# Kernel optimization log

Hardware: AMD Instinct MI355X
Metric: run time of the kernel (lower is better)

## Reference

```python
import jax, jax.numpy as jnp
import numpy as np

N = 50000      # nodes
E = 600000     # edges (avg degree 12)
D_IN = 16      # node_input_size
D = 128        # hidden_size
H = 4          # num_heads
DH = D // H
L = 4          # message_passing_num
D_FF = 512     # 4*hidden FFN expansion
D_OUT = 3      # output_size


def setup_inputs() -> dict:
    key = jax.random.key(0)
    ks = iter(jax.random.split(key, 32))
    def w(shape, fan_in):
        return jax.random.normal(next(ks), shape, jnp.float32) / np.float32(np.sqrt(fan_in))
    return {
        "features": jax.random.normal(next(ks), (N, D_IN), jnp.float32),
        "senders": jax.random.randint(next(ks), (E,), 0, N),
        "receivers": jax.random.randint(next(ks), (E,), 0, N),
        "enc_w1": w((D_IN, D), D_IN), "enc_b1": jnp.zeros((D,), jnp.float32),
        "enc_w2": w((D, D), D),       "enc_b2": jnp.zeros((D,), jnp.float32),
        "wq": w((L, D, D), D), "wk": w((L, D, D), D),
        "wv": w((L, D, D), D), "wo": w((L, D, D), D),
        "ln1_s": jnp.ones((L, D), jnp.float32), "ln1_b": jnp.zeros((L, D), jnp.float32),
        "ffn_w1": w((L, D, D_FF), D), "ffn_b1": jnp.zeros((L, D_FF), jnp.float32),
        "ffn_w2": w((L, D_FF, D), D_FF), "ffn_b2": jnp.zeros((L, D), jnp.float32),
        "ln2_s": jnp.ones((L, D), jnp.float32), "ln2_b": jnp.zeros((L, D), jnp.float32),
        "dec_w1": w((D, D_OUT), D), "dec_b1": jnp.zeros((D_OUT,), jnp.float32),
        "dec_w2": w((D_OUT, D_OUT), D_OUT), "dec_b2": jnp.zeros((D_OUT,), jnp.float32),
    }


def _ln(x, s, b):
    mu = x.mean(-1, keepdims=True)
    var = ((x - mu) ** 2).mean(-1, keepdims=True)
    return (x - mu) * jax.lax.rsqrt(var + 1e-5) * s + b


def _graph_mha(x, senders, receivers, wq, wk, wv, wo):
    # Adjacency-masked attention done sparsely over the edge list
    # (equivalent to softmax over the BCOO adjacency pattern).
    n = x.shape[0]
    q = (x @ wq).reshape(n, H, DH)
    k = (x @ wk).reshape(n, H, DH)
    v = (x @ wv).reshape(n, H, DH)
    scores = (q[receivers] * k[senders]).sum(-1) / np.float32(np.sqrt(DH))  # [E,H]
    m = jax.ops.segment_max(scores, receivers, num_segments=n)             # [N,H]
    m = jnp.where(jnp.isfinite(m), m, 0.0)
    a = jnp.exp(scores - m[receivers])                                      # [E,H]
    denom = jax.ops.segment_sum(a, receivers, num_segments=n)              # [N,H]
    msg = jax.ops.segment_sum(a[:, :, None] * v[senders], receivers, num_segments=n)  # [N,H,DH]
    out = (msg / (denom[:, :, None] + 1e-9)).reshape(n, D)
    return out @ wo


def reference(features, senders, receivers,
              enc_w1, enc_b1, enc_w2, enc_b2,
              wq, wk, wv, wo, ln1_s, ln1_b,
              ffn_w1, ffn_b1, ffn_w2, ffn_b2, ln2_s, ln2_b,
              dec_w1, dec_b1, dec_w2, dec_b2):
    # encode
    x = jnp.maximum(features @ enc_w1 + enc_b1, 0.0) @ enc_w2 + enc_b2     # [N,D]
    # process: L pre-LN sparse-attention transformer blocks
    for l in range(L):
        h = _ln(x, ln1_s[l], ln1_b[l])
        x = x + _graph_mha(h, senders, receivers, wq[l], wk[l], wv[l], wo[l])
        h = _ln(x, ln2_s[l], ln2_b[l])
        x = x + jnp.maximum(h @ ffn_w1[l] + ffn_b1[l], 0.0) @ ffn_w2[l] + ffn_b2[l]
    # decode
    return jnp.maximum(x @ dec_w1 + dec_b1, 0.0) @ dec_w2 + dec_b2         # [N,D_OUT]
```

## Files before the change

kernel.cpp:

```cpp
#include <hip/hip_runtime.h>
#include <hip/hip_bf16.h>
#include <math.h>

#define D     128
#define NHEAD 4
#define DH    32
#define DFF   512
#define DIN   16
#define MAXDEG 64
#define TN    16

typedef __attribute__((ext_vector_type(8))) short bf16x8;
typedef __attribute__((ext_vector_type(4))) float f32x4;
typedef __hip_bfloat16 bf16;

#define QSCALE_L2E 0.2550348838f

#define BMQ 128

#define WAITV(N) asm volatile("s_waitcnt vmcnt(" #N ")" ::: "memory")
#define WAITLGKM asm volatile("s_waitcnt lgkmcnt(0)" ::: "memory")
#define FENCE()  asm volatile("" ::: "memory")
#define BAR() do { FENCE(); __builtin_amdgcn_s_barrier(); FENCE(); } while (0)

__device__ __forceinline__ void gll16(const bf16* g, bf16* l) {
    __builtin_amdgcn_global_load_lds((__attribute__((address_space(1))) void*)g,
                                     (__attribute__((address_space(3))) void*)l,
                                     16, 0, 0);
}

__device__ __forceinline__ ushort bfbits(float f) {
    __hip_bfloat16 b = __float2bfloat16(f);
    return *(ushort*)&b;
}

__global__ void k_fill(const int* __restrict__ recv, const int* __restrict__ senders,
                       int* __restrict__ deg, int* __restrict__ eid, int E) {
    int e = blockIdx.x * blockDim.x + threadIdx.x;
    if (e >= E) return;
    int r = recv[e];
    int pos = atomicAdd(&deg[r], 1);
    if (pos < MAXDEG) eid[r * MAXDEG + pos] = senders[e];
}

__global__ void k_wt(const float* __restrict__ wq, const float* __restrict__ wk,
                     const float* __restrict__ wv, const float* __restrict__ wo,
                     const float* __restrict__ w1, const float* __restrict__ w2,
                     const float* __restrict__ encw2,
                     bf16* __restrict__ wqkvT, bf16* __restrict__ woT,
                     bf16* __restrict__ w1T, bf16* __restrict__ w2T,
                     bf16* __restrict__ encw2T, int* __restrict__ deg,
                     int* __restrict__ eid, int N) {
    int r = blockIdx.y;
    if (r == 25) {
        int tot = N + N * MAXDEG;
        for (int i = blockIdx.x * blockDim.x + threadIdx.x; i < tot;
             i += 256 * 256) {
            if (i < N) deg[i] = 0;
            else eid[i - N] = 0;
        }
        return;
    }
    const float* src; bf16* dst; int K, Nout;
    if (r < 12) {
        int l = r / 3, sel = r % 3;
        src = (sel == 0 ? wq : sel == 1 ? wk : wv) + (size_t)l * D * D;
        dst = wqkvT + (size_t)l * 3 * D * D + (size_t)sel * D * D;
        K = D; Nout = D;
    } else if (r < 16) {
        int l = r - 12;
        src = wo + (size_t)l * D * D; dst = woT + (size_t)l * D * D; K = D; Nout = D;
    } else if (r < 20) {
        int l = r - 16;
        src = w1 + (size_t)l * D * DFF; dst = w1T + (size_t)l * D * DFF; K = D; Nout = DFF;
    } else if (r < 24) {
        int l = r - 20;
        src = w2 + (size_t)l * DFF * D; dst = w2T + (size_t)l * DFF * D; K = DFF; Nout = D;
    } else {
        src = encw2; dst = encw2T; K = D; Nout = D;
    }
    int total = K * Nout;
    int i = blockIdx.x * blockDim.x + threadIdx.x;
    if (i >= total) return;
    int k = i / Nout, j = i % Nout;
    dst[(size_t)j * K + k] = __float2bfloat16(src[i]);
}

__device__ __forceinline__ void load_afrag(const bf16* A, int arow, int quad,
                                           int N, bf16x8* afr) {
    const bf16* ab = A + (size_t)arow * D + quad * 8;
#pragma unroll
    for (int i = 0; i < 4; i++) {
        uint4 v = make_uint4(0u, 0u, 0u, 0u);
        if (arow < N) v = *(const uint4*)(ab + i * 32);
        afr[i] = *(bf16x8*)&v;
    }
}

__device__ __forceinline__ void stage_full256(bf16* lb, const bf16* src,
                                              int wave, int lane) {
#pragma unroll
    for (int k = 0; k < 8; k++) {
        int gidx = (wave * 8 + k) * 64 + lane;
        int r = gidx >> 4, gL = gidx & 15;
        gll16(src + (size_t)r * 128 + ((gL ^ (r & 15)) * 8),
              lb + (size_t)(wave * 8 + k) * 512);
    }
}

__device__ __forceinline__ void stage_full512(bf16* lb, const bf16* src,
                                              int wave, int lane) {
#pragma unroll
    for (int k = 0; k < 4; k++) {
        int gidx = (wave * 4 + k) * 64 + lane;
        int r = gidx >> 4, gL = gidx & 15;
        gll16(src + (size_t)r * 128 + ((gL ^ (r & 15)) * 8),
              lb + (size_t)(wave * 4 + k) * 512);
    }
}

__device__ __forceinline__ void stage_q(bf16* lb, const bf16* src, int rs,
                                        int wave, int lane) {
#pragma unroll
    for (int k = 0; k < 2; k++) {
        int gidx = (wave * 2 + k) * 64 + lane;
        int r = gidx >> 2, gL = gidx & 3;
        gll16(src + (size_t)r * rs + ((gL ^ ((r >> 1) & 3)) * 8),
              lb + (size_t)(wave * 2 + k) * 512);
    }
}

__device__ __forceinline__ void mfma_tile(const bf16* Wb, const bf16x8* afr,
                                          f32x4* acc, int l16, int quad) {
#pragma unroll
    for (int i = 0; i < 4; i++)
#pragma unroll
        for (int j = 0; j < 8; j++) {
            const bf16* wp = Wb + (size_t)(j * 16 + l16) * 128
                              + (size_t)((((i * 4 + quad)) ^ l16) * 8);
            acc[j] = __builtin_amdgcn_mfma_f32_16x16x32_bf16(afr[i], *(const bf16x8*)wp,
                                                             acc[j], 0, 0, 0);
        }
}

template<int OP>
__global__ __launch_bounds__(256) void k_gemm(
        const bf16* __restrict__ A, const bf16* __restrict__ Bt,
        const float* __restrict__ bias,
        const float* __restrict__ lns, const float* __restrict__ lnb,
        float* x, bf16* outB, int N) {
    __shared__ alignas(16) bf16 Wsm[128 * 128];
    int m0 = blockIdx.x * 64;
    int t = threadIdx.x;
    int wave = t >> 6, lane = t & 63;
    int quad = lane >> 4, l16 = lane & 15;
    int wm = wave * 16;

    bf16x8 afr[4];
    load_afrag(A, m0 + wm + l16, quad, N, afr);
    FENCE();
    stage_full256(Wsm, Bt, wave, lane);
    WAITV(0); BAR();

    int rowb = m0 + wm + quad * 4;
    float xv[8][4];
    if (OP == 2) {
#pragma unroll
        for (int j = 0; j < 8; j++)
#pragma unroll
            for (int r = 0; r < 4; r++) {
                int gr = rowb + r;
                xv[j][r] = (gr < N) ? x[(size_t)gr * D + j * 16 + l16] : 0.f;
            }
    }

    f32x4 acc[8];
#pragma unroll
    for (int j = 0; j < 8; j++) acc[j] = (f32x4){0.f, 0.f, 0.f, 0.f};
    mfma_tile(Wsm, afr, acc, l16, quad);

    float bv[8];
    if (OP == 5) {
#pragma unroll
        for (int j = 0; j < 8; j++) bv[j] = bias[j * 16 + l16];
    }
#pragma unroll
    for (int j = 0; j < 8; j++) {
#pragma unroll
        for (int r = 0; r < 4; r++) {
            int gr = rowb + r;
            if (gr >= N) continue;
            float val = acc[j][r];
            if (OP == 5) val += bv[j];
            if (OP == 2) val += xv[j][r];
            acc[j][r] = val;
        }
    }
    float lsv[8], lbv[8];
#pragma unroll
    for (int j = 0; j < 8; j++) {
        lsv[j] = lns[j * 16 + l16];
        lbv[j] = lnb[j * 16 + l16];
    }
#pragma unroll
    for (int r = 0; r < 4; r++) {
        float s1 = 0.f, s2 = 0.f;
#pragma unroll
        for (int j = 0; j < 8; j++) {
            float v = acc[j][r];
            s1 += v; s2 += v * v;
        }
        s1 += __shfl_xor(s1, 1, 64);  s2 += __shfl_xor(s2, 1, 64);
        s1 += __shfl_xor(s1, 2, 64);  s2 += __shfl_xor(s2, 2, 64);
        s1 += __shfl_xor(s1, 4, 64);  s2 += __shfl_xor(s2, 4, 64);
        s1 += __shfl_xor(s1, 8, 64);  s2 += __shfl_xor(s2, 8, 64);
        float mu = s1 * (1.f / 128.f);
        float var = s2 * (1.f / 128.f) - mu * mu;
        float rinv = rsqrtf(fmaxf(var, 0.f) + 1e-5f);
        int gr = rowb + r;
        if (gr >= N) continue;
#pragma unroll
        for (int j = 0; j < 8; j++) {
            int col = j * 16 + l16;
            float v = acc[j][r];
            x[(size_t)gr * D + col] = v;
            outB[(size_t)gr * D + col] =
                __float2bfloat16((v - mu) * rinv * lsv[j] + lbv[j]);
        }
    }
}

__global__ __launch_bounds__(512, 2) void k_qkv(
        const bf16* __restrict__ hb, const bf16* __restrict__ wqkvT,
        bf16* __restrict__ qb, bf16* __restrict__ kvb, int N) {
    __shared__ alignas(16) bf16 Wbuf[2][128 * 128];
    int m0 = blockIdx.x * BMQ;
    int t = threadIdx.x;
    int wave = t >> 6, lane = t & 63;
    int quad = lane >> 4, l16 = lane & 15;
    int wm = wave * 16;

    bf16x8 afr[4];
    load_afrag(hb, m0 + wm + l16, quad, N, afr);
    FENCE();
    stage_full512(Wbuf[0], wqkvT + (size_t)D * D, wave, lane);
    FENCE();
    stage_full512(Wbuf[1], wqkvT + (size_t)2 * D * D, wave, lane);
    FENCE();

    int rowb = m0 + wm + quad * 4;
    f32x4 ak[8], acc[8];
#pragma unroll
    for (int j = 0; j < 8; j++) ak[j] = (f32x4){0.f, 0.f, 0.f, 0.f};

    WAITV(4); BAR();
    __builtin_amdgcn_s_setprio(1);
    mfma_tile(Wbuf[0], afr, ak, l16, quad);
    __builtin_amdgcn_s_setprio(0);
    BAR();
    stage_full512(Wbuf[0], wqkvT, wave, lane);
    FENCE();
#pragma unroll
    for (int j = 0; j < 8; j++) acc[j] = (f32x4){0.f, 0.f, 0.f, 0.f};
    WAITV(4); BAR();
    __builtin_amdgcn_s_setprio(1);
    mfma_tile(Wbuf[1], afr, acc, l16, quad);
    __builtin_amdgcn_s_setprio(0);

#pragma unroll
    for (int j = 0; j < 8; j++) {
        int col = j * 16 + l16;
#pragma unroll
        for (int r = 0; r < 4; r++) {
            int gr = rowb + r;
            if (gr >= N) continue;
            uint kv = (uint)bfbits(ak[j][r]) | ((uint)bfbits(acc[j][r]) << 16);
            *(uint*)&kvb[((size_t)gr * D + col) * 2] = kv;
        }
    }
    FENCE();
    if (m0 + BMQ <= N) { WAITV(32); } else { WAITV(0); }
    BAR();
#pragma unroll
    for (int j = 0; j < 8; j++) acc[j] = (f32x4){0.f, 0.f, 0.f, 0.f};
    __builtin_amdgcn_s_setprio(1);
    mfma_tile(Wbuf[0], afr, acc, l16, quad);
    __builtin_amdgcn_s_setprio(0);
#pragma unroll
    for (int j = 0; j < 8; j++) {
        int col = j * 16 + l16;
#pragma unroll
        for (int r = 0; r < 4; r++) {
            int gr = rowb + r;
            if (gr >= N) continue;
            qb[(size_t)gr * D + col] = __float2bfloat16(acc[j][r] * QSCALE_L2E);
        }
    }
}

__device__ __forceinline__ void stage_ffn_q(int ts, const bf16* w1T,
                                            const bf16* w2T, bf16* Wb6,
                                            int wave, int lane) {
    int c = ts >> 3, p = ts & 7;
    const bf16* src; int rs;
    if (p < 4) { src = w1T + (size_t)(c * 128) * 128 + p * 32;       rs = 128; }
    else       { src = w2T + (size_t)(c * 128) + (p - 4) * 32;       rs = DFF; }
    stage_q(Wb6 + (size_t)(ts % 6) * (32 * 128), src, rs, wave, lane);
}

template<int MODE>
__global__ __launch_bounds__(256) void k_ffn(
        const bf16* __restrict__ hb, const bf16* __restrict__ w1T,
        const float* __restrict__ b1,
        const bf16* __restrict__ w2T, const float* __restrict__ b2,
        const float* __restrict__ lns, const float* __restrict__ lnb,
        const float* __restrict__ dw1, const float* __restrict__ db1,
        const float* __restrict__ dw2, const float* __restrict__ db2,
        float* x, bf16* outB, float* out, int N) {
    __shared__ alignas(16) bf16 Wb6[6][32 * 128];
    __shared__ alignas(16) bf16 Hsm[64 * 128];
    int m0 = blockIdx.x * 64;
    int t = threadIdx.x;
    int wave = t >> 6, lane = t & 63;
    int quad = lane >> 4, l16 = lane & 15;
    int wm = wave * 16;
    int rowb = m0 + wm + quad * 4;

    float b1pre[4][8];
#pragma unroll
    for (int c2 = 0; c2 < 4; c2++)
#pragma unroll
        for (int j = 0; j < 8; j++) b1pre[c2][j] = b1[c2 * 128 + j * 16 + l16];

    bf16x8 afr[4];
    load_afrag(hb, m0 + wm + l16, quad, N, afr);
    FENCE();
    stage_ffn_q(0, w1T, w2T, &Wb6[0][0], wave, lane); FENCE();
    stage_ffn_q(1, w1T, w2T, &Wb6[0][0], wave, lane); FENCE();
    stage_ffn_q(2, w1T, w2T, &Wb6[0][0], wave, lane); FENCE();
    stage_ffn_q(3, w1T, w2T, &Wb6[0][0], wave, lane); FENCE();

    f32x4 acc2[8], accP[8];
#pragma unroll
    for (int j = 0; j < 8; j++) acc2[j] = (f32x4){0.f, 0.f, 0.f, 0.f};
    float xv[8][4];

    int wswz = (quad ^ ((l16 >> 1) & 3)) * 8;

#pragma unroll
    for (int s = 0; s < 32; s++) {
        if (s + 4 < 32) {
            stage_ffn_q(s + 4, w1T, w2T, &Wb6[0][0], wave, lane);
            FENCE();
        }
        if (s < 28)       { WAITV(8); }
        else if (s == 28) { WAITV(6); }
        else if (s == 29) { WAITV(4); }
        else if (s == 30) { WAITV(2); }
        else              { WAITV(0); }
        BAR();
        if (s == 31) {
#pragma unroll
            for (int j = 0; j < 8; j++)
#pragma unroll
                for (int r = 0; r < 4; r++) {
                    int gr = min(rowb + r, N - 1);
                    xv[j][r] = x[(size_t)gr * D + j * 16 + l16];
                }
            FENCE();
        }
        const bf16* Wb = &Wb6[0][0] + (size_t)(s % 6) * (32 * 128);
        int c = s >> 3, p = s & 7;
        if (p < 4) {
            if (p == 0) {
#pragma unroll
                for (int j = 0; j < 8; j++) accP[j] = (f32x4){0.f, 0.f, 0.f, 0.f};
            }
            __builtin_amdgcn_s_setprio(1);
#pragma unroll
            for (int j = 0; j < 8; j++) {
                const bf16* wp = Wb + (size_t)(j * 16 + l16) * 32 + wswz;
                accP[j] = __builtin_amdgcn_mfma_f32_16x16x32_bf16(
                    afr[p], *(const bf16x8*)wp, accP[j], 0, 0, 0);
            }
            __builtin_amdgcn_s_setprio(0);
            if (p == 3) {
                int rw = wm + quad * 4;
#pragma unroll
                for (int j = 0; j < 8; j++) {
                    int gb = j * 2 + (l16 >> 3), ce = l16 & 7;
#pragma unroll
                    for (int r = 0; r < 4; r++) {
                        int row = rw + r;
                        Hsm[(size_t)row * 128 + (size_t)((gb ^ (row & 15)) * 8) + ce] =
                            __float2bfloat16(fmaxf(accP[j][r] + b1pre[c][j], 0.f));
                    }
                }
                WAITLGKM;
            }
        } else {
            int kq = p - 4;
            bf16x8 af2 = *(const bf16x8*)(Hsm + (size_t)(wm + l16) * 128
                              + (size_t)(((kq * 4 + quad) ^ l16) * 8));
            __builtin_amdgcn_s_setprio(1);
#pragma unroll
            for (int j = 0; j < 8; j++) {
                const bf16* wp = Wb + (size_t)(j * 16 + l16) * 32 + wswz;
                acc2[j] = __builtin_amdgcn_mfma_f32_16x16x32_bf16(
                    af2, *(const bf16x8*)wp, acc2[j], 0, 0, 0);
            }
            __builtin_amdgcn_s_setprio(0);
        }
    }
    WAITV(0);
    FENCE();

    float bv[8];
#pragma unroll
    for (int j = 0; j < 8; j++) bv[j] = b2[j * 16 + l16];
#pragma unroll
    for (int j = 0; j < 8; j++) {
#pragma unroll
        for (int r = 0; r < 4; r++) {
            int gr = rowb + r;
            if (gr >= N) continue;
            acc2[j][r] += bv[j] + xv[j][r];
        }
    }
    if (MODE == 1) {
        float dw[8][3];
#pragma unroll
        for (int j = 0; j < 8; j++) {
            int col = j * 16 + l16;
#pragma unroll
            for (int cc3 = 0; cc3 < 3; cc3++) dw[j][cc3] = dw1[col * 3 + cc3];
        }
#pragma unroll
        for (int r = 0; r < 4; r++) {
            float s0 = 0.f, s1 = 0.f, s2 = 0.f;
#pragma unroll
            for (int j = 0; j < 8; j++) {
                float v = acc2[j][r];
                s0 += v * dw[j][0]; s1 += v * dw[j][1]; s2 += v * dw[j][2];
            }
            s0 += __shfl_xor(s0, 1, 64); s1 += __shfl_xor(s1, 1, 64); s2 += __shfl_xor(s2, 1, 64);
            s0 += __shfl_xor(s0, 2, 64); s1 += __shfl_xor(s1, 2, 64); s2 += __shfl_xor(s2, 2, 64);
            s0 += __shfl_xor(s0, 4, 64); s1 += __shfl_xor(s1, 4, 64); s2 += __shfl_xor(s2, 4, 64);
            s0 += __shfl_xor(s0, 8, 64); s1 += __shfl_xor(s1, 8, 64); s2 += __shfl_xor(s2, 8, 64);
            int gr = rowb + r;
            if (l16 == 0 && gr < N) {
                float t0 = fmaxf(s0 + db1[0], 0.f);
                float t1 = fmaxf(s1 + db1[1], 0.f);
                float t2 = fmaxf(s2 + db1[2], 0.f);
#pragma unroll
                for (int o = 0; o < 3; o++)
                    out[(size_t)gr * 3 + o] =
                        t0 * dw2[0 * 3 + o] + t1 * dw2[1 * 3 + o] + t2 * dw2[2 * 3 + o] + db2[o];
            }
        }
        return;
    }
    float lsv[8], lbv[8];
#pragma unroll
    for (int j = 0; j < 8; j++) {
        lsv[j] = lns[j * 16 + l16];
        lbv[j] = lnb[j * 16 + l16];
    }
#pragma unroll
    for (int r = 0; r < 4; r++) {
        float s1 = 0.f, s2 = 0.f;
#pragma unroll
        for (int j = 0; j < 8; j++) {
            float v = acc2[j][r];
            s1 += v; s2 += v * v;
        }
        s1 += __shfl_xor(s1, 1, 64);  s2 += __shfl_xor(s2, 1, 64);
        s1 += __shfl_xor(s1, 2, 64);  s2 += __shfl_xor(s2, 2, 64);
        s1 += __shfl_xor(s1, 4, 64);  s2 += __shfl_xor(s2, 4, 64);
        s1 += __shfl_xor(s1, 8, 64);  s2 += __shfl_xor(s2, 8, 64);
        float mu = s1 * (1.f / 128.f);
        float var = s2 * (1.f / 128.f) - mu * mu;
        float rinv = rsqrtf(fmaxf(var, 0.f) + 1e-5f);
        int gr = rowb + r;
        if (gr >= N) continue;
#pragma unroll
        for (int j = 0; j < 8; j++) {
            int col = j * 16 + l16;
            float v = acc2[j][r];
            x[(size_t)gr * D + col] = v;
            outB[(size_t)gr * D + col] = __float2bfloat16((v - mu) * rinv * lsv[j] + lbv[j]);
        }
    }
}

__global__ void k_enc1(const float* __restrict__ feat,
                       const float* __restrict__ w1, const float* __restrict__ b1,
                       bf16* __restrict__ hb, int N) {
    __shared__ float fsh[TN][DIN];
    int n0 = blockIdx.x * TN;
    int j = threadIdx.x;
    int nvalid = min(TN, N - n0);
    for (int idx = j; idx < TN * DIN; idx += 128) {
        int n = idx / DIN, i = idx % DIN;
        fsh[n][i] = (n < nvalid) ? feat[(n0 + n) * DIN + i] : 0.f;
    }
    __syncthreads();
    float bb = b1[j];
#pragma unroll
    for (int n = 0; n < TN; n++) {
        float a = bb;
#pragma unroll
        for (int i = 0; i < DIN; i++) a += fsh[n][i] * w1[i * D + j];
        if (n < nvalid) hb[(size_t)(n0 + n) * D + j] = __float2bfloat16(fmaxf(a, 0.f));
    }
}

__device__ __forceinline__ void attn_edge(uint4 w, bool v, float4 qv,
                                          float& l, float& a0, float& a1,
                                          float& a2, float& a3) {
    float k0 = __uint_as_float(w.x << 16), v0 = __uint_as_float(w.x & 0xFFFF0000u);
    float k1 = __uint_as_float(w.y << 16), v1 = __uint_as_float(w.y & 0xFFFF0000u);
    float k2 = __uint_as_float(w.z << 16), v2 = __uint_as_float(w.z & 0xFFFF0000u);
    float k3 = __uint_as_float(w.w << 16), v3 = __uint_as_float(w.w & 0xFFFF0000u);
    float p = qv.x * k0 + qv.y * k1 + qv.z * k2 + qv.w * k3;
    p += __shfl_xor(p, 1, 64);
    p += __shfl_xor(p, 2, 64);
    p += __shfl_xor(p, 4, 64);
    float e = v ? exp2f(p) : 0.f;
    l += e;
    a0 += e * v0; a1 += e * v1; a2 += e * v2; a3 += e * v3;
}

__device__ __forceinline__ float4 unpackq(uint2 qw) {
    float4 qv;
    qv.x = __uint_as_float(qw.x << 16);
    qv.y = __uint_as_float(qw.x & 0xFFFF0000u);
    qv.z = __uint_as_float(qw.y << 16);
    qv.w = __uint_as_float(qw.y & 0xFFFF0000u);
    return qv;
}

__global__ __launch_bounds__(256) void k_attn(
        const bf16* __restrict__ qb, const uint* __restrict__ kvb,
        const int* __restrict__ deg, const int* __restrict__ eid,
        bf16* __restrict__ out, int N) {
    int wave = threadIdx.x >> 6, lane = threadIdx.x & 63;
    int g = lane & 7, h = (lane >> 3) & 3, slot = lane >> 5;
    int d0 = h * 32 + g * 4;
    int rbase = blockIdx.x * 16 + wave * 4;
    if (rbase >= N) return;
    const uint* kvbase = kvb + d0;

    int ssN[8];
    {
        const int* row = eid + (size_t)rbase * MAXDEG;
#pragma unroll
        for (int u = 0; u < 8; u++) ssN[u] = row[u * 2 + slot];
    }
    int cntN = min(deg[rbase], MAXDEG);
    float4 qvN = unpackq(*(const uint2*)(qb + (size_t)rbase * D + d0));

#pragma unroll
    for (int i = 0; i < 4; i++) {
        int r = rbase + i;
        if (r >= N) return;
        int cnt = cntN; float4 qv = qvN;
        uint4 w[8];
#pragma unroll
        for (int u = 0; u < 8; u++)
            w[u] = *(const uint4*)(kvbase + (size_t)ssN[u] * D);
        int rn = r + 1;
        if (i < 3 && rn < N) {
            const int* rowN = eid + (size_t)rn * MAXDEG;
#pragma unroll
            for (int u = 0; u < 8; u++) ssN[u] = rowN[u * 2 + slot];
            cntN = min(deg[rn], MAXDEG);
            qvN = unpackq(*(const uint2*)(qb + (size_t)rn * D + d0));
        }
        float l = 0.f, a0 = 0.f, a1 = 0.f, a2 = 0.f, a3 = 0.f;
#pragma unroll
        for (int u = 0; u < 8; u++)
            attn_edge(w[u], (u * 2 + slot) < cnt, qv, l, a0, a1, a2, a3);
        for (int base = 16; base < cnt; base += 16) {
            const int* row = eid + (size_t)r * MAXDEG;
            int ss[8]; bool vv[8];
#pragma unroll
            for (int u = 0; u < 8; u++) {
                int e = base + u * 2 + slot;
                vv[u] = e < cnt;
                ss[u] = row[e];
            }
            uint4 w2_[8];
#pragma unroll
            for (int u = 0; u < 8; u++)
                w2_[u] = *(const uint4*)(kvbase + (size_t)ss[u] * D);
#pragma unroll
            for (int u = 0; u < 8; u++)
                attn_edge(w2_[u], vv[u], qv, l, a0, a1, a2, a3);
        }
        l  += __shfl_xor(l, 32, 64);
        a0 += __shfl_xor(a0, 32, 64);
        a1 += __shfl_xor(a1, 32, 64);
        a2 += __shfl_xor(a2, 32, 64);
        a3 += __shfl_xor(a3, 32, 64);
        if (lane < 32) {
            float inv = 1.f / (l + 1e-9f);
            bf16 o[4];
            o[0] = __float2bfloat16(a0 * inv);
            o[1] = __float2bfloat16(a1 * inv);
            o[2] = __float2bfloat16(a2 * inv);
            o[3] = __float2bfloat16(a3 * inv);
            *(uint2*)(out + (size_t)r * D + d0) = *(uint2*)o;
        }
    }
}

extern "C" void kernel_launch(void* const* d_in, const int* in_sizes, int n_in,
                              void* d_out, int out_size, void* d_ws, size_t ws_size,
                              hipStream_t stream) {
    const float* feat    = (const float*)d_in[0];
    const int*   senders = (const int*)d_in[1];
    const int*   recv    = (const int*)d_in[2];
    const float* enc_w1  = (const float*)d_in[3];
    const float* enc_b1  = (const float*)d_in[4];
    const float* enc_w2  = (const float*)d_in[5];
    const float* enc_b2  = (const float*)d_in[6];
    const float* wq      = (const float*)d_in[7];
    const float* wk      = (const float*)d_in[8];
    const float* wv      = (const float*)d_in[9];
    const float* wo      = (const float*)d_in[10];
    const float* ln1_s   = (const float*)d_in[11];
    const float* ln1_b   = (const float*)d_in[12];
    const float* ffn_w1  = (const float*)d_in[13];
    const float* ffn_b1  = (const float*)d_in[14];
    const float* ffn_w2  = (const float*)d_in[15];
    const float* ffn_b2  = (const float*)d_in[16];
    const float* ln2_s   = (const float*)d_in[17];
    const float* ln2_b   = (const float*)d_in[18];
    const float* dec_w1  = (const float*)d_in[19];
    const float* dec_b1  = (const float*)d_in[20];
    const float* dec_w2  = (const float*)d_in[21];
    const float* dec_b2  = (const float*)d_in[22];

    int N = in_sizes[0] / DIN;
    int E = in_sizes[1];

    char* p = (char*)d_ws;
    float* x   = (float*)p;  p += (size_t)N * D * 4;
    bf16*  qb  = (bf16*)p;   p += (size_t)N * D * 2;
    bf16*  kvb = (bf16*)p;   p += (size_t)N * D * 2 * 2;
    bf16*  hb  = (bf16*)p;   p += (size_t)N * D * 2;
    int* deg   = (int*)p;    p += (size_t)N * 4;
    int* eid   = (int*)p;    p += (size_t)N * MAXDEG * 4;
    bf16* wqkvT  = (bf16*)p; p += (size_t)4 * 3 * D * D * 2;
    bf16* woT    = (bf16*)p; p += (size_t)4 * D * D * 2;
    bf16* w1T    = (bf16*)p; p += (size_t)4 * D * DFF * 2;
    bf16* w2T    = (bf16*)p; p += (size_t)4 * DFF * D * 2;
    bf16* encw2T = (bf16*)p; p += (size_t)D * D * 2;

    int gm64 = (N + 63) / 64;
    int gmQ  = (N + BMQ - 1) / BMQ;

    k_wt<<<dim3(256, 26), 256, 0, stream>>>(wq, wk, wv, wo, ffn_w1, ffn_w2, enc_w2,
                                            wqkvT, woT, w1T, w2T, encw2T, deg, eid, N);
    k_fill<<<(E + 255) / 256, 256, 0, stream>>>(recv, senders, deg, eid, E);
    k_enc1<<<(N + TN - 1) / TN, 128, 0, stream>>>(feat, enc_w1, enc_b1, hb, N);
    k_gemm<5><<<gm64, 256, 0, stream>>>(hb, encw2T, enc_b2, ln1_s, ln1_b, x, hb, N);

    for (int l = 0; l < 4; l++) {
        k_qkv<<<gmQ, 512, 0, stream>>>(hb, wqkvT + (size_t)l * 3 * D * D, qb, kvb, N);
        k_attn<<<(N + 15) / 16, 256, 0, stream>>>(qb, (const uint*)kvb, deg, eid, hb, N);
        k_gemm<2><<<gm64, 256, 0, stream>>>(hb, woT + (size_t)l * D * D,
                                            nullptr, ln2_s + l * D, ln2_b + l * D,
                                            x, hb, N);
        if (l < 3)
            k_ffn<0><<<gm64, 256, 0, stream>>>(hb, w1T + (size_t)l * D * DFF,
                                               ffn_b1 + l * DFF,
                                               w2T + (size_t)l * DFF * D, ffn_b2 + l * D,
                                               ln1_s + (l + 1) * D, ln1_b + (l + 1) * D,
                                               nullptr, nullptr, nullptr, nullptr,
                                               x, hb, nullptr, N);
        else
            k_ffn<1><<<gm64, 256, 0, stream>>>(hb, w1T + (size_t)l * D * DFF,
                                               ffn_b1 + l * DFF,
                                               w2T + (size_t)l * DFF * D, ffn_b2 + l * D,
                                               nullptr, nullptr,
                                               dec_w1, dec_b1, dec_w2, dec_b2,
                                               x, nullptr, (float*)d_out, N);
    }
}
```

Baseline: 619.3 us.

## Stream weights in 32-column K-slices with ring buffer for QKV and output GEMMs

Both the QKV projection and the output/encoder GEMM now stage their weight matrix in 32-wide K-slices. The slices go through a 6-slot LDS ring in k_qkv and 4 slots in k_gemm, with graded vmcnt waits, so MFMA work on early slices overlaps loads of later ones instead of waiting for the full 128x128 tile. k_qkv drops from 512-thread, 128-row blocks to 256-thread, 64-row blocks with smaller shared memory, which should raise occupancy but re-reads the weights more often across blocks. It also adds a barrier per slice.

```diff
diff --git a/kernel.cpp b/kernel.cpp
--- a/kernel.cpp
+++ b/kernel.cpp
@@ -16,7 +16,6 @@
 
 #define QSCALE_L2E 0.2550348838f
 
-#define BMQ 128
 
 #define WAITV(N) asm volatile("s_waitcnt vmcnt(" #N ")" ::: "memory")
 #define WAITLGKM asm volatile("s_waitcnt lgkmcnt(0)" ::: "memory")
@@ -97,28 +96,6 @@
     }
 }
 
-__device__ __forceinline__ void stage_full256(bf16* lb, const bf16* src,
-                                              int wave, int lane) {
-#pragma unroll
-    for (int k = 0; k < 8; k++) {
-        int gidx = (wave * 8 + k) * 64 + lane;
-        int r = gidx >> 4, gL = gidx & 15;
-        gll16(src + (size_t)r * 128 + ((gL ^ (r & 15)) * 8),
-              lb + (size_t)(wave * 8 + k) * 512);
-    }
-}
-
-__device__ __forceinline__ void stage_full512(bf16* lb, const bf16* src,
-                                              int wave, int lane) {
-#pragma unroll
-    for (int k = 0; k < 4; k++) {
-        int gidx = (wave * 4 + k) * 64 + lane;
-        int r = gidx >> 4, gL = gidx & 15;
-        gll16(src + (size_t)r * 128 + ((gL ^ (r & 15)) * 8),
-              lb + (size_t)(wave * 4 + k) * 512);
-    }
-}
-
 __device__ __forceinline__ void stage_q(bf16* lb, const bf16* src, int rs,
                                         int wave, int lane) {
 #pragma unroll
@@ -128,19 +105,6 @@
         gll16(src + (size_t)r * rs + ((gL ^ ((r >> 1) & 3)) * 8),
               lb + (size_t)(wave * 2 + k) * 512);
     }
-}
-
-__device__ __forceinline__ void mfma_tile(const bf16* Wb, const bf16x8* afr,
-                                          f32x4* acc, int l16, int quad) {
-#pragma unroll
-    for (int i = 0; i < 4; i++)
-#pragma unroll
-        for (int j = 0; j < 8; j++) {
-            const bf16* wp = Wb + (size_t)(j * 16 + l16) * 128
-                              + (size_t)((((i * 4 + quad)) ^ l16) * 8);
-            acc[j] = __builtin_amdgcn_mfma_f32_16x16x32_bf16(afr[i], *(const bf16x8*)wp,
-                                                             acc[j], 0, 0, 0);
-        }
 }
 
 template<int OP>
@@ -149,35 +113,52 @@
         const float* __restrict__ bias,
         const float* __restrict__ lns, const float* __restrict__ lnb,
         float* x, bf16* outB, int N) {
-    __shared__ alignas(16) bf16 Wsm[128 * 128];
+    __shared__ alignas(16) bf16 Wq4[4][32 * 128];
     int m0 = blockIdx.x * 64;
     int t = threadIdx.x;
     int wave = t >> 6, lane = t & 63;
     int quad = lane >> 4, l16 = lane & 15;
     int wm = wave * 16;
-
+    int rowb = m0 + wm + quad * 4;
+
+    float xv[8][4];
+    if (OP == 2) {
+#pragma unroll
+        for (int j = 0; j < 8; j++)
+#pragma unroll
+            for (int r = 0; r < 4; r++) {
+                int gr = rowb + r;
+                xv[j][r] = (gr < N) ? x[(size_t)gr * D + j * 16 + l16] : 0.f;
+            }
+    }
     bf16x8 afr[4];
     load_afrag(A, m0 + wm + l16, quad, N, afr);
     FENCE();
-    stage_full256(Wsm, Bt, wave, lane);
-    WAITV(0); BAR();
-
-    int rowb = m0 + wm + quad * 4;
-    float xv[8][4];
-    if (OP == 2) {
-#pragma unroll
-        for (int j = 0; j < 8; j++)
-#pragma unroll
-            for (int r = 0; r < 4; r++) {
-                int gr = rowb + r;
-                xv[j][r] = (gr < N) ? x[(size_t)gr * D + j * 16 + l16] : 0.f;
-            }
-    }
-
+#pragma unroll
+    for (int p = 0; p < 4; p++) {
+        stage_q(&Wq4[p][0], Bt + p * 32, 128, wave, lane);
+        FENCE();
+    }
+
+    int wswz = (quad ^ ((l16 >> 1) & 3)) * 8;
     f32x4 acc[8];
 #pragma unroll
     for (int j = 0; j < 8; j++) acc[j] = (f32x4){0.f, 0.f, 0.f, 0.f};
-    mfma_tile(Wsm, afr, acc, l16, quad);
+#pragma unroll
+    for (int s = 0; s < 4; s++) {
+        if (s == 0) { WAITV(6); } else if (s == 1) { WAITV(4); }
+        else if (s == 2) { WAITV(2); } else { WAITV(0); }
+        BAR();
+        const bf16* Wb = &Wq4[s][0];
+        __builtin_amdgcn_s_setprio(1);
+#pragma unroll
+        for (int j = 0; j < 8; j++) {
+            const bf16* wp = Wb + (size_t)(j * 16 + l16) * 32 + wswz;
+            acc[j] = __builtin_amdgcn_mfma_f32_16x16x32_bf16(
+                afr[s], *(const bf16x8*)wp, acc[j], 0, 0, 0);
+        }
+        __builtin_amdgcn_s_setprio(0);
+    }
 
     float bv[8];
     if (OP == 5) {
@@ -230,42 +211,71 @@
     }
 }
 
-__global__ __launch_bounds__(512, 2) void k_qkv(
+__device__ __forceinline__ void stage_qkv_q(int ts, const bf16* wqkvT,
+                                            bf16* Wb6, int wave, int lane) {
+    int tsel = ts >> 2, p = ts & 3;
+    size_t off = (tsel == 0) ? (size_t)D * D
+               : (tsel == 1) ? (size_t)2 * D * D : 0;
+    stage_q(Wb6 + (size_t)(ts % 6) * (32 * 128), wqkvT + off + p * 32, 128,
+            wave, lane);
+}
+
+__global__ __launch_bounds__(256) void k_qkv(
         const bf16* __restrict__ hb, const bf16* __restrict__ wqkvT,
         bf16* __restrict__ qb, bf16* __restrict__ kvb, int N) {
-    __shared__ alignas(16) bf16 Wbuf[2][128 * 128];
-    int m0 = blockIdx.x * BMQ;
+    __shared__ alignas(16) bf16 Wb6[6][32 * 128];
+    int m0 = blockIdx.x * 64;
     int t = threadIdx.x;
     int wave = t >> 6, lane = t & 63;
     int quad = lane >> 4, l16 = lane & 15;
     int wm = wave * 16;
+    int rowb = m0 + wm + quad * 4;
 
     bf16x8 afr[4];
     load_afrag(hb, m0 + wm + l16, quad, N, afr);
     FENCE();
-    stage_full512(Wbuf[0], wqkvT + (size_t)D * D, wave, lane);
-    FENCE();
-    stage_full512(Wbuf[1], wqkvT + (size_t)2 * D * D, wave, lane);
-    FENCE();
-
-    int rowb = m0 + wm + quad * 4;
-    f32x4 ak[8], acc[8];
-#pragma unroll
-    for (int j = 0; j < 8; j++) ak[j] = (f32x4){0.f, 0.f, 0.f, 0.f};
-
-    WAITV(4); BAR();
-    __builtin_amdgcn_s_setprio(1);
-    mfma_tile(Wbuf[0], afr, ak, l16, quad);
-    __builtin_amdgcn_s_setprio(0);
-    BAR();
-    stage_full512(Wbuf[0], wqkvT, wave, lane);
-    FENCE();
-#pragma unroll
-    for (int j = 0; j < 8; j++) acc[j] = (f32x4){0.f, 0.f, 0.f, 0.f};
-    WAITV(4); BAR();
-    __builtin_amdgcn_s_setprio(1);
-    mfma_tile(Wbuf[1], afr, acc, l16, quad);
-    __builtin_amdgcn_s_setprio(0);
+    stage_qkv_q(0, wqkvT, &Wb6[0][0], wave, lane); FENCE();
+    stage_qkv_q(1, wqkvT, &Wb6[0][0], wave, lane); FENCE();
+    stage_qkv_q(2, wqkvT, &Wb6[0][0], wave, lane); FENCE();
+    stage_qkv_q(3, wqkvT, &Wb6[0][0], wave, lane); FENCE();
+
+    int wswz = (quad ^ ((l16 >> 1) & 3)) * 8;
+    f32x4 accK[8], accV[8], accQ[8];
+
+#pragma unroll
+    for (int s = 0; s < 12; s++) {
+        if (s + 4 < 12) {
+            stage_qkv_q(s + 4, wqkvT, &Wb6[0][0], wave, lane);
+            FENCE();
+        }
+        if (s < 8)        { WAITV(8); }
+        else if (s == 8)  { WAITV(6); }
+        else if (s == 9)  { WAITV(4); }
+        else if (s == 10) { WAITV(2); }
+        else              { WAITV(0); }
+        BAR();
+        const bf16* Wb = &Wb6[0][0] + (size_t)(s % 6) * (32 * 128);
+        int q = s & 3;
+        __builtin_amdgcn_s_setprio(1);
+#pragma unroll
+        for (int j = 0; j < 8; j++) {
+            const bf16* wp = Wb + (size_t)(j * 16 + l16) * 32 + wswz;
+            if (s < 4) {
+                if (q == 0) accK[j] = (f32x4){0.f, 0.f, 0.f, 0.f};
+                accK[j] = __builtin_amdgcn_mfma_f32_16x16x32_bf16(
+                    afr[q], *(const bf16x8*)wp, accK[j], 0, 0, 0);
+            } else if (s < 8) {
+                if (q == 0) accV[j] = (f32x4){0.f, 0.f, 0.f, 0.f};
+                accV[j] = __builtin_amdgcn_mfma_f32_16x16x32_bf16(
+                    afr[q], *(const bf16x8*)wp, accV[j], 0, 0, 0);
+            } else {
+                if (q == 0) accQ[j] = (f32x4){0.f, 0.f, 0.f, 0.f};
+                accQ[j] = __builtin_amdgcn_mfma_f32_16x16x32_bf16(
+                    afr[q], *(const bf16x8*)wp, accQ[j], 0, 0, 0);
+            }
+        }
+        __builtin_amdgcn_s_setprio(0);
+    }
 
 #pragma unroll
     for (int j = 0; j < 8; j++) {
@@ -274,26 +284,9 @@
         for (int r = 0; r < 4; r++) {
             int gr = rowb + r;
             if (gr >= N) continue;
-            uint kv = (uint)bfbits(ak[j][r]) | ((uint)bfbits(acc[j][r]) << 16);
+            uint kv = (uint)bfbits(accK[j][r]) | ((uint)bfbits(accV[j][r]) << 16);
             *(uint*)&kvb[((size_t)gr * D + col) * 2] = kv;
-        }
-    }
-    FENCE();
-    if (m0 + BMQ <= N) { WAITV(32); } else { WAITV(0); }
-    BAR();
-#pragma unroll
-    for (int j = 0; j < 8; j++) acc[j] = (f32x4){0.f, 0.f, 0.f, 0.f};
-    __builtin_amdgcn_s_setprio(1);
-    mfma_tile(Wbuf[0], afr, acc, l16, quad);
-    __builtin_amdgcn_s_setprio(0);
-#pragma unroll
-    for (int j = 0; j < 8; j++) {
-        int col = j * 16 + l16;
-#pragma unroll
-        for (int r = 0; r < 4; r++) {
-            int gr = rowb + r;
-            if (gr >= N) continue;
-            qb[(size_t)gr * D + col] = __float2bfloat16(acc[j][r] * QSCALE_L2E);
+            qb[(size_t)gr * D + col] = __float2bfloat16(accQ[j][r] * QSCALE_L2E);
         }
     }
 }
@@ -659,7 +652,6 @@
     bf16* encw2T = (bf16*)p; p += (size_t)D * D * 2;
 
     int gm64 = (N + 63) / 64;
-    int gmQ  = (N + BMQ - 1) / BMQ;
 
     k_wt<<<dim3(256, 26), 256, 0, stream>>>(wq, wk, wv, wo, ffn_w1, ffn_w2, enc_w2,
                                             wqkvT, woT, w1T, w2T, encw2T, deg, eid, N);
@@ -668,7 +660,7 @@
     k_gemm<5><<<gm64, 256, 0, stream>>>(hb, encw2T, enc_b2, ln1_s, ln1_b, x, hb, N);
 
     for (int l = 0; l < 4; l++) {
-        k_qkv<<<gmQ, 512, 0, stream>>>(hb, wqkvT + (size_t)l * 3 * D * D, qb, kvb, N);
+        k_qkv<<<gm64, 256, 0, stream>>>(hb, wqkvT + (size_t)l * 3 * D * D, qb, kvb, N);
         k_attn<<<(N + 15) / 16, 256, 0, stream>>>(qb, (const uint*)kvb, deg, eid, hb, N);
         k_gemm<2><<<gm64, 256, 0, stream>>>(hb, woT + (size_t)l * D * D,
                                             nullptr, ln2_s + l * D, ln2_b + l * D,
```

New measurement: 636.3 us. +2.8%, slower.
